# Kernel optimization log

Hardware: AMD Instinct MI355X
Metric: run time of the kernel (lower is better)

The kernel has to match this reference:

```python
import jax, jax.numpy as jnp
import numpy as np

B, H, NQ, NK, D = 256, 16, 49, 49, 64
SCALE = 1.0 / np.sqrt(D).astype(np.float32)
EPS = 1e-9  # matches kernel's 1/(l + 1e-9)


def setup_inputs() -> dict:
    key = jax.random.key(0)
    kq, kk, kv = jax.random.split(key, 3)
    q = jax.random.normal(kq, (B, H, NQ, D), dtype=jnp.float32)
    k = jax.random.normal(kk, (B, H, NK, D), dtype=jnp.float32)
    v = jax.random.normal(kv, (B, H, NK, D), dtype=jnp.float32)
    return {"q": q, "k": k, "v": v}


def reference(q, k, v):
    # scores: [B,H,Nq,Nk]
    s = jnp.einsum("bhqd,bhkd->bhqk", q, k) * SCALE
    m = jnp.max(s, axis=-1, keepdims=True)
    e = jnp.exp(s - m)
    l = jnp.sum(e, axis=-1, keepdims=True)
    p = e / (l + EPS)  # kernel divides by (l + 1e-9)
    out = jnp.einsum("bhqk,bhkd->bhqd", p, v)
    return out
```

## Files before the change

### kernel.cpp

```cpp
#include <hip/hip_runtime.h>


#define NQA 49
#define DD  64
#define ST  72

typedef __bf16 bf16x4 __attribute__((ext_vector_type(4)));
typedef __bf16 bf16x8 __attribute__((ext_vector_type(8)));
typedef float  f32x4  __attribute__((ext_vector_type(4)));

__device__ __forceinline__ int vt_off(int d, int k) {
    return d * ST + ((((k >> 3) + ((d >> 2) & 7)) & 7) << 3) + (k & 7);
}

__global__ __launch_bounds__(256, 5)
void attn49_kernel(const float* __restrict__ Q, const float* __restrict__ K,
                   const float* __restrict__ V, float* __restrict__ O) {
    __shared__ __bf16 Qs[64 * ST];
    __shared__ __bf16 Ks[64 * ST];
    __shared__ __bf16 Vt[64 * ST];

    const int tid = threadIdx.x;
    const size_t base = (size_t)blockIdx.x * (NQA * DD);
    const float* Qg = Q + base;
    const float* Kg = K + base;
    const float* Vg = V + base;

    {
        const int f  = tid & 15;
        const int r0 = tid >> 4;
        #pragma unroll
        for (int it = 0; it < 4; ++it) {
            const int r = r0 + 16 * it;
            float4 qv = {0.f,0.f,0.f,0.f}, kv = {0.f,0.f,0.f,0.f},
                   vv = {0.f,0.f,0.f,0.f};
            if (r < NQA) {
                qv = *(const float4*)(Qg + r * DD + 4 * f);
                kv = *(const float4*)(Kg + r * DD + 4 * f);
                vv = *(const float4*)(Vg + r * DD + 4 * f);
            }
            bf16x4 qb = { (__bf16)(0.125f*qv.x), (__bf16)(0.125f*qv.y),
                          (__bf16)(0.125f*qv.z), (__bf16)(0.125f*qv.w) };
            bf16x4 kb = { (__bf16)kv.x, (__bf16)kv.y, (__bf16)kv.z, (__bf16)kv.w };
            *(bf16x4*)&Qs[r * ST + 4 * f] = qb;
            *(bf16x4*)&Ks[r * ST + 4 * f] = kb;
            Vt[vt_off(4*f + 0, r)] = (__bf16)vv.x;
            Vt[vt_off(4*f + 1, r)] = (__bf16)vv.y;
            Vt[vt_off(4*f + 2, r)] = (__bf16)vv.z;
            Vt[vt_off(4*f + 3, r)] = (__bf16)vv.w;
        }
    }
    __syncthreads();

    const int w  = tid >> 6;
    const int lr = tid & 15;
    const int lg = (tid >> 4) & 3;

    bf16x8 aq0 = *(const bf16x8*)&Qs[(16*w + lr) * ST      + 8*lg];
    bf16x8 aq1 = *(const bf16x8*)&Qs[(16*w + lr) * ST + 32 + 8*lg];
    f32x4 acc[4] = {};
    #pragma unroll
    for (int t = 0; t < 4; ++t) {
        bf16x8 b0 = *(const bf16x8*)&Ks[(16*t + lr) * ST      + 8*lg];
        bf16x8 b1 = *(const bf16x8*)&Ks[(16*t + lr) * ST + 32 + 8*lg];
        acc[t] = __builtin_amdgcn_mfma_f32_16x16x32_bf16(aq0, b0, acc[t], 0, 0, 0);
        acc[t] = __builtin_amdgcn_mfma_f32_16x16x32_bf16(aq1, b1, acc[t], 0, 0, 0);
    }

    float inv_l[4];
    #pragma unroll
    for (int i = 0; i < 4; ++i) {
        const int gq = 16*w + 4*lg + i;
        float e0 = __expf(acc[0][i]);
        float e1 = __expf(acc[1][i]);
        float e2 = __expf(acc[2][i]);
        float e3 = (lr == 0) ? __expf(acc[3][i]) : 0.f;
        float sum = (e0 + e1) + (e2 + e3);
        #pragma unroll
        for (int d = 1; d < 16; d <<= 1) sum += __shfl_xor(sum, d, 64);
        inv_l[i] = 1.f / (sum + 1e-9f);
        Qs[gq * ST +  0 + lr] = (__bf16)e0;
        Qs[gq * ST + 16 + lr] = (__bf16)e1;
        Qs[gq * ST + 32 + lr] = (__bf16)e2;
        Qs[gq * ST + 48 + lr] = (__bf16)e3;
    }

    bf16x8 ap0 = *(const bf16x8*)&Qs[(16*w + lr) * ST      + 8*lg];
    bf16x8 ap1 = *(const bf16x8*)&Qs[(16*w + lr) * ST + 32 + 8*lg];
    f32x4 oacc[4] = {};
    #pragma unroll
    for (int t = 0; t < 4; ++t) {
        bf16x8 b0 = *(const bf16x8*)&Vt[vt_off(16*t + lr,  8*lg)];
        bf16x8 b1 = *(const bf16x8*)&Vt[vt_off(16*t + lr, 32 + 8*lg)];
        oacc[t] = __builtin_amdgcn_mfma_f32_16x16x32_bf16(ap0, b0, oacc[t], 0, 0, 0);
        oacc[t] = __builtin_amdgcn_mfma_f32_16x16x32_bf16(ap1, b1, oacc[t], 0, 0, 0);
    }

    float* Og = O + base;
    #pragma unroll
    for (int i = 0; i < 4; ++i) {
        const int gq = 16*w + 4*lg + i;
        if (gq < NQA) {
            #pragma unroll
            for (int t = 0; t < 4; ++t)
                Og[gq * DD + 16*t + lr] = oacc[t][i] * inv_l[i];
        }
    }
}

extern "C" void kernel_launch(void* const* d_in, const int* in_sizes, int n_in,
                              void* d_out, int out_size, void* d_ws, size_t ws_size,
                              hipStream_t stream) {
    const float* q = (const float*)d_in[0];
    const float* k = (const float*)d_in[1];
    const float* v = (const float*)d_in[2];
    float* out = (float*)d_out;
    (void)in_sizes; (void)n_in; (void)out_size; (void)d_ws; (void)ws_size;
    attn49_kernel<<<dim3(4096), dim3(256), 0, stream>>>(q, k, v, out);
}
```

Measured before the change: 186.4 us.

## Load Q directly into MFMA registers and reuse K buffer for probabilities

Q is now read from global memory straight into the MFMA A-operand registers instead of being staged through shared memory. The K shared buffer is reused for the exponentiated scores after a new barrier. This cuts LDS per block from three tiles to two, and the launch bound is raised from 5 to 8 blocks per CU to turn the saved LDS into higher occupancy. The cost is an extra __syncthreads and per-lane strided global Q loads that are less coalesced than before.

```diff
diff --git a/kernel.cpp b/kernel.cpp
--- a/kernel.cpp
+++ b/kernel.cpp
@@ -13,16 +13,14 @@
     return d * ST + ((((k >> 3) + ((d >> 2) & 7)) & 7) << 3) + (k & 7);
 }
 
-__global__ __launch_bounds__(256, 5)
+__global__ __launch_bounds__(256, 8)
 void attn49_kernel(const float* __restrict__ Q, const float* __restrict__ K,
                    const float* __restrict__ V, float* __restrict__ O) {
-    __shared__ __bf16 Qs[64 * ST];
-    __shared__ __bf16 Ks[64 * ST];
+    __shared__ __bf16 KPs[64 * ST];
     __shared__ __bf16 Vt[64 * ST];
 
     const int tid = threadIdx.x;
     const size_t base = (size_t)blockIdx.x * (NQA * DD);
-    const float* Qg = Q + base;
     const float* Kg = K + base;
     const float* Vg = V + base;
 
@@ -32,40 +30,57 @@
         #pragma unroll
         for (int it = 0; it < 4; ++it) {
             const int r = r0 + 16 * it;
-            float4 qv = {0.f,0.f,0.f,0.f}, kv = {0.f,0.f,0.f,0.f},
-                   vv = {0.f,0.f,0.f,0.f};
+            float4 kv = {0.f,0.f,0.f,0.f}, vv = {0.f,0.f,0.f,0.f};
             if (r < NQA) {
-                qv = *(const float4*)(Qg + r * DD + 4 * f);
                 kv = *(const float4*)(Kg + r * DD + 4 * f);
                 vv = *(const float4*)(Vg + r * DD + 4 * f);
             }
-            bf16x4 qb = { (__bf16)(0.125f*qv.x), (__bf16)(0.125f*qv.y),
-                          (__bf16)(0.125f*qv.z), (__bf16)(0.125f*qv.w) };
             bf16x4 kb = { (__bf16)kv.x, (__bf16)kv.y, (__bf16)kv.z, (__bf16)kv.w };
-            *(bf16x4*)&Qs[r * ST + 4 * f] = qb;
-            *(bf16x4*)&Ks[r * ST + 4 * f] = kb;
+            *(bf16x4*)&KPs[r * ST + 4 * f] = kb;
             Vt[vt_off(4*f + 0, r)] = (__bf16)vv.x;
             Vt[vt_off(4*f + 1, r)] = (__bf16)vv.y;
             Vt[vt_off(4*f + 2, r)] = (__bf16)vv.z;
             Vt[vt_off(4*f + 3, r)] = (__bf16)vv.w;
         }
     }
-    __syncthreads();
 
     const int w  = tid >> 6;
     const int lr = tid & 15;
     const int lg = (tid >> 4) & 3;
 
-    bf16x8 aq0 = *(const bf16x8*)&Qs[(16*w + lr) * ST      + 8*lg];
-    bf16x8 aq1 = *(const bf16x8*)&Qs[(16*w + lr) * ST + 32 + 8*lg];
+    bf16x8 aq0, aq1;
+    {
+        const int qrow = 16*w + lr;
+        float4 qa = {0.f,0.f,0.f,0.f}, qb = {0.f,0.f,0.f,0.f},
+               qc = {0.f,0.f,0.f,0.f}, qd = {0.f,0.f,0.f,0.f};
+        if (qrow < NQA) {
+            const float* Qr = Q + base + (size_t)qrow * DD + 8 * lg;
+            qa = *(const float4*)(Qr +  0);
+            qb = *(const float4*)(Qr +  4);
+            qc = *(const float4*)(Qr + 32);
+            qd = *(const float4*)(Qr + 36);
+        }
+        aq0 = bf16x8{ (__bf16)(0.125f*qa.x), (__bf16)(0.125f*qa.y),
+                      (__bf16)(0.125f*qa.z), (__bf16)(0.125f*qa.w),
+                      (__bf16)(0.125f*qb.x), (__bf16)(0.125f*qb.y),
+                      (__bf16)(0.125f*qb.z), (__bf16)(0.125f*qb.w) };
+        aq1 = bf16x8{ (__bf16)(0.125f*qc.x), (__bf16)(0.125f*qc.y),
+                      (__bf16)(0.125f*qc.z), (__bf16)(0.125f*qc.w),
+                      (__bf16)(0.125f*qd.x), (__bf16)(0.125f*qd.y),
+                      (__bf16)(0.125f*qd.z), (__bf16)(0.125f*qd.w) };
+    }
+    __syncthreads();
+
     f32x4 acc[4] = {};
     #pragma unroll
     for (int t = 0; t < 4; ++t) {
-        bf16x8 b0 = *(const bf16x8*)&Ks[(16*t + lr) * ST      + 8*lg];
-        bf16x8 b1 = *(const bf16x8*)&Ks[(16*t + lr) * ST + 32 + 8*lg];
+        bf16x8 b0 = *(const bf16x8*)&KPs[(16*t + lr) * ST      + 8*lg];
+        bf16x8 b1 = *(const bf16x8*)&KPs[(16*t + lr) * ST + 32 + 8*lg];
         acc[t] = __builtin_amdgcn_mfma_f32_16x16x32_bf16(aq0, b0, acc[t], 0, 0, 0);
         acc[t] = __builtin_amdgcn_mfma_f32_16x16x32_bf16(aq1, b1, acc[t], 0, 0, 0);
     }
+
+    __syncthreads();
 
     float inv_l[4];
     #pragma unroll
@@ -79,14 +94,14 @@
         #pragma unroll
         for (int d = 1; d < 16; d <<= 1) sum += __shfl_xor(sum, d, 64);
         inv_l[i] = 1.f / (sum + 1e-9f);
-        Qs[gq * ST +  0 + lr] = (__bf16)e0;
-        Qs[gq * ST + 16 + lr] = (__bf16)e1;
-        Qs[gq * ST + 32 + lr] = (__bf16)e2;
-        Qs[gq * ST + 48 + lr] = (__bf16)e3;
+        KPs[gq * ST +  0 + lr] = (__bf16)e0;
+        KPs[gq * ST + 16 + lr] = (__bf16)e1;
+        KPs[gq * ST + 32 + lr] = (__bf16)e2;
+        KPs[gq * ST + 48 + lr] = (__bf16)e3;
     }
 
-    bf16x8 ap0 = *(const bf16x8*)&Qs[(16*w + lr) * ST      + 8*lg];
-    bf16x8 ap1 = *(const bf16x8*)&Qs[(16*w + lr) * ST + 32 + 8*lg];
+    bf16x8 ap0 = *(const bf16x8*)&KPs[(16*w + lr) * ST      + 8*lg];
+    bf16x8 ap1 = *(const bf16x8*)&KPs[(16*w + lr) * ST + 32 + 8*lg];
     f32x4 oacc[4] = {};
     #pragma unroll
     for (int t = 0; t < 4; ++t) {
```

Result: no change. 184.9 us (-0.8%).

## Process four heads per block with double-buffered LDS and register prefetch

Applied to the files above, without the earlier changes.

Each block now handles four heads instead of one, and the grid shrinks to a quarter. Global loads for the next head are issued into registers while the current head computes, with K/V staged into alternating LDS buffers. Q is loaded straight into MFMA operand registers, so the Q shared buffer is gone and P is written into the K buffer after a barrier. The point is to hide global load latency and cut per-block launch and setup overhead, at the cost of higher register pressure and fewer concurrent blocks (launch bounds drop from 5 to 4).

```diff
diff --git a/kernel.cpp b/kernel.cpp
--- a/kernel.cpp
+++ b/kernel.cpp
@@ -4,6 +4,7 @@
 #define NQA 49
 #define DD  64
 #define ST  72
+#define HPB 4
 
 typedef __bf16 bf16x4 __attribute__((ext_vector_type(4)));
 typedef __bf16 bf16x8 __attribute__((ext_vector_type(8)));
@@ -13,59 +14,82 @@
     return d * ST + ((((k >> 3) + ((d >> 2) & 7)) & 7) << 3) + (k & 7);
 }
 
-__global__ __launch_bounds__(256, 5)
-void attn49_kernel(const float* __restrict__ Q, const float* __restrict__ K,
-                   const float* __restrict__ V, float* __restrict__ O) {
-    __shared__ __bf16 Qs[64 * ST];
-    __shared__ __bf16 Ks[64 * ST];
-    __shared__ __bf16 Vt[64 * ST];
+__device__ __forceinline__ void lds_barrier() {
+    asm volatile("s_waitcnt lgkmcnt(0)" ::: "memory");
+    __builtin_amdgcn_s_barrier();
+}
 
-    const int tid = threadIdx.x;
-    const size_t base = (size_t)blockIdx.x * (NQA * DD);
-    const float* Qg = Q + base;
+struct Pref {
+    float4 kr[4], vr[4];
+    float4 qa, qb, qc, qd;
+};
+
+__device__ __forceinline__ void issue_loads(const float* __restrict__ Q,
+                                            const float* __restrict__ K,
+                                            const float* __restrict__ V,
+                                            size_t head, int f, int r0,
+                                            int w, int lr, int lg, Pref& p) {
+    const size_t base = head * (size_t)(NQA * DD);
     const float* Kg = K + base;
     const float* Vg = V + base;
-
-    {
-        const int f  = tid & 15;
-        const int r0 = tid >> 4;
-        #pragma unroll
-        for (int it = 0; it < 4; ++it) {
-            const int r = r0 + 16 * it;
-            float4 qv = {0.f,0.f,0.f,0.f}, kv = {0.f,0.f,0.f,0.f},
-                   vv = {0.f,0.f,0.f,0.f};
-            if (r < NQA) {
-                qv = *(const float4*)(Qg + r * DD + 4 * f);
-                kv = *(const float4*)(Kg + r * DD + 4 * f);
-                vv = *(const float4*)(Vg + r * DD + 4 * f);
-            }
-            bf16x4 qb = { (__bf16)(0.125f*qv.x), (__bf16)(0.125f*qv.y),
-                          (__bf16)(0.125f*qv.z), (__bf16)(0.125f*qv.w) };
-            bf16x4 kb = { (__bf16)kv.x, (__bf16)kv.y, (__bf16)kv.z, (__bf16)kv.w };
-            *(bf16x4*)&Qs[r * ST + 4 * f] = qb;
-            *(bf16x4*)&Ks[r * ST + 4 * f] = kb;
-            Vt[vt_off(4*f + 0, r)] = (__bf16)vv.x;
-            Vt[vt_off(4*f + 1, r)] = (__bf16)vv.y;
-            Vt[vt_off(4*f + 2, r)] = (__bf16)vv.z;
-            Vt[vt_off(4*f + 3, r)] = (__bf16)vv.w;
+    #pragma unroll
+    for (int it = 0; it < 4; ++it) {
+        const int r = r0 + 16 * it;
+        p.kr[it] = float4{0.f, 0.f, 0.f, 0.f};
+        p.vr[it] = float4{0.f, 0.f, 0.f, 0.f};
+        if (r < NQA) {
+            p.kr[it] = *(const float4*)(Kg + r * DD + 4 * f);
+            p.vr[it] = *(const float4*)(Vg + r * DD + 4 * f);
         }
     }
-    __syncthreads();
+    const int qrow = 16 * w + lr;
+    p.qa = p.qb = p.qc = p.qd = float4{0.f, 0.f, 0.f, 0.f};
+    if (qrow < NQA) {
+        const float* Qr = Q + base + (size_t)qrow * DD + 8 * lg;
+        p.qa = *(const float4*)(Qr + 0);
+        p.qb = *(const float4*)(Qr + 4);
+        p.qc = *(const float4*)(Qr + 32);
+        p.qd = *(const float4*)(Qr + 36);
+    }
+}
 
-    const int w  = tid >> 6;
-    const int lr = tid & 15;
-    const int lg = (tid >> 4) & 3;
+__device__ __forceinline__ void stage(const Pref& p, __bf16* Ksb, __bf16* Vtb,
+                                      int f, int r0, bf16x8& aq0, bf16x8& aq1) {
+    #pragma unroll
+    for (int it = 0; it < 4; ++it) {
+        const int r = r0 + 16 * it;
+        bf16x4 kb = { (__bf16)p.kr[it].x, (__bf16)p.kr[it].y,
+                      (__bf16)p.kr[it].z, (__bf16)p.kr[it].w };
+        *(bf16x4*)&Ksb[r * ST + 4 * f] = kb;
+        Vtb[vt_off(4*f + 0, r)] = (__bf16)p.vr[it].x;
+        Vtb[vt_off(4*f + 1, r)] = (__bf16)p.vr[it].y;
+        Vtb[vt_off(4*f + 2, r)] = (__bf16)p.vr[it].z;
+        Vtb[vt_off(4*f + 3, r)] = (__bf16)p.vr[it].w;
+    }
+    aq0 = bf16x8{ (__bf16)(0.125f*p.qa.x), (__bf16)(0.125f*p.qa.y),
+                  (__bf16)(0.125f*p.qa.z), (__bf16)(0.125f*p.qa.w),
+                  (__bf16)(0.125f*p.qb.x), (__bf16)(0.125f*p.qb.y),
+                  (__bf16)(0.125f*p.qb.z), (__bf16)(0.125f*p.qb.w) };
+    aq1 = bf16x8{ (__bf16)(0.125f*p.qc.x), (__bf16)(0.125f*p.qc.y),
+                  (__bf16)(0.125f*p.qc.z), (__bf16)(0.125f*p.qc.w),
+                  (__bf16)(0.125f*p.qd.x), (__bf16)(0.125f*p.qd.y),
+                  (__bf16)(0.125f*p.qd.z), (__bf16)(0.125f*p.qd.w) };
+}
 
-    bf16x8 aq0 = *(const bf16x8*)&Qs[(16*w + lr) * ST      + 8*lg];
-    bf16x8 aq1 = *(const bf16x8*)&Qs[(16*w + lr) * ST + 32 + 8*lg];
+__device__ __forceinline__ void compute_head(float* __restrict__ O, size_t head,
+                                             __bf16* Ksb, const __bf16* Vtb,
+                                             bf16x8 aq0, bf16x8 aq1,
+                                             int w, int lr, int lg) {
     f32x4 acc[4] = {};
     #pragma unroll
     for (int t = 0; t < 4; ++t) {
-        bf16x8 b0 = *(const bf16x8*)&Ks[(16*t + lr) * ST      + 8*lg];
-        bf16x8 b1 = *(const bf16x8*)&Ks[(16*t + lr) * ST + 32 + 8*lg];
+        bf16x8 b0 = *(const bf16x8*)&Ksb[(16*t + lr) * ST      + 8*lg];
+        bf16x8 b1 = *(const bf16x8*)&Ksb[(16*t + lr) * ST + 32 + 8*lg];
         acc[t] = __builtin_amdgcn_mfma_f32_16x16x32_bf16(aq0, b0, acc[t], 0, 0, 0);
         acc[t] = __builtin_amdgcn_mfma_f32_16x16x32_bf16(aq1, b1, acc[t], 0, 0, 0);
     }
+
+    lds_barrier();
 
     float inv_l[4];
     #pragma unroll
@@ -79,24 +103,24 @@
         #pragma unroll
         for (int d = 1; d < 16; d <<= 1) sum += __shfl_xor(sum, d, 64);
         inv_l[i] = 1.f / (sum + 1e-9f);
-        Qs[gq * ST +  0 + lr] = (__bf16)e0;
-        Qs[gq * ST + 16 + lr] = (__bf16)e1;
-        Qs[gq * ST + 32 + lr] = (__bf16)e2;
-        Qs[gq * ST + 48 + lr] = (__bf16)e3;
+        Ksb[gq * ST +  0 + lr] = (__bf16)e0;
+        Ksb[gq * ST + 16 + lr] = (__bf16)e1;
+        Ksb[gq * ST + 32 + lr] = (__bf16)e2;
+        Ksb[gq * ST + 48 + lr] = (__bf16)e3;
     }
 
-    bf16x8 ap0 = *(const bf16x8*)&Qs[(16*w + lr) * ST      + 8*lg];
-    bf16x8 ap1 = *(const bf16x8*)&Qs[(16*w + lr) * ST + 32 + 8*lg];
+    bf16x8 ap0 = *(const bf16x8*)&Ksb[(16*w + lr) * ST      + 8*lg];
+    bf16x8 ap1 = *(const bf16x8*)&Ksb[(16*w + lr) * ST + 32 + 8*lg];
     f32x4 oacc[4] = {};
     #pragma unroll
     for (int t = 0; t < 4; ++t) {
-        bf16x8 b0 = *(const bf16x8*)&Vt[vt_off(16*t + lr,  8*lg)];
-        bf16x8 b1 = *(const bf16x8*)&Vt[vt_off(16*t + lr, 32 + 8*lg)];
+        bf16x8 b0 = *(const bf16x8*)&Vtb[vt_off(16*t + lr,  8*lg)];
+        bf16x8 b1 = *(const bf16x8*)&Vtb[vt_off(16*t + lr, 32 + 8*lg)];
         oacc[t] = __builtin_amdgcn_mfma_f32_16x16x32_bf16(ap0, b0, oacc[t], 0, 0, 0);
         oacc[t] = __builtin_amdgcn_mfma_f32_16x16x32_bf16(ap1, b1, oacc[t], 0, 0, 0);
     }
 
-    float* Og = O + base;
+    float* Og = O + head * (size_t)(NQA * DD);
     #pragma unroll
     for (int i = 0; i < 4; ++i) {
         const int gq = 16*w + 4*lg + i;
@@ -108,6 +132,46 @@
     }
 }
 
+__global__ __launch_bounds__(256, 4)
+void attn49_kernel(const float* __restrict__ Q, const float* __restrict__ K,
+                   const float* __restrict__ V, float* __restrict__ O) {
+    __shared__ __bf16 Ks[2][64 * ST];
+    __shared__ __bf16 Vt[2][64 * ST];
+
+    const int tid = threadIdx.x;
+    const int f  = tid & 15;
+    const int r0 = tid >> 4;
+    const int w  = tid >> 6;
+    const int lr = tid & 15;
+    const int lg = (tid >> 4) & 3;
+
+    const size_t h0 = (size_t)blockIdx.x * HPB;
+
+    Pref p;
+    bf16x8 aqA0, aqA1, aqB0, aqB1;
+
+    issue_loads(Q, K, V, h0 + 0, f, r0, w, lr, lg, p);
+    stage(p, Ks[0], Vt[0], f, r0, aqA0, aqA1);
+    issue_loads(Q, K, V, h0 + 1, f, r0, w, lr, lg, p);
+    lds_barrier();
+
+    compute_head(O, h0 + 0, Ks[0], Vt[0], aqA0, aqA1, w, lr, lg);
+    stage(p, Ks[1], Vt[1], f, r0, aqB0, aqB1);
+    issue_loads(Q, K, V, h0 + 2, f, r0, w, lr, lg, p);
+    lds_barrier();
+
+    compute_head(O, h0 + 1, Ks[1], Vt[1], aqB0, aqB1, w, lr, lg);
+    stage(p, Ks[0], Vt[0], f, r0, aqA0, aqA1);
+    issue_loads(Q, K, V, h0 + 3, f, r0, w, lr, lg, p);
+    lds_barrier();
+
+    compute_head(O, h0 + 2, Ks[0], Vt[0], aqA0, aqA1, w, lr, lg);
+    stage(p, Ks[1], Vt[1], f, r0, aqB0, aqB1);
+    lds_barrier();
+
+    compute_head(O, h0 + 3, Ks[1], Vt[1], aqB0, aqB1, w, lr, lg);
+}
+
 extern "C" void kernel_launch(void* const* d_in, const int* in_sizes, int n_in,
                               void* d_out, int out_size, void* d_ws, size_t ws_size,
                               hipStream_t stream) {
@@ -116,5 +180,5 @@
     const float* v = (const float*)d_in[2];
     float* out = (float*)d_out;
     (void)in_sizes; (void)n_in; (void)out_size; (void)d_ws; (void)ws_size;
-    attn49_kernel<<<dim3(4096), dim3(256), 0, stream>>>(q, k, v, out);
+    attn49_kernel<<<dim3(4096 / HPB), dim3(256), 0, stream>>>(q, k, v, out);
 }
```

After: 190.3 us. 2.1% more time.

## Load Q/K/V directly into MFMA registers, drop shared-memory staging and barrier

Applied to the files above, without the earlier changes.

Replaces block-wide shared-memory staging of Q, K and transposed V with per-wave direct global loads converted into bf16 MFMA operands, keeping only a small per-wave LDS tile for the probability matrix. This removes the block barrier and LDS traffic and lowers shared memory per block. In exchange each wave re-reads all of K and V from global/L2 and V is gathered with scalar strided loads. Launch bounds are also changed to target 4 blocks per SIMD.

```diff
diff --git a/kernel.cpp b/kernel.cpp
--- a/kernel.cpp
+++ b/kernel.cpp
@@ -3,107 +3,114 @@
 
 #define NQA 49
 #define DD  64
-#define ST  72
+#define PST 72
 
-typedef __bf16 bf16x4 __attribute__((ext_vector_type(4)));
 typedef __bf16 bf16x8 __attribute__((ext_vector_type(8)));
 typedef float  f32x4  __attribute__((ext_vector_type(4)));
 
-__device__ __forceinline__ int vt_off(int d, int k) {
-    return d * ST + ((((k >> 3) + ((d >> 2) & 7)) & 7) << 3) + (k & 7);
-}
-
-__global__ __launch_bounds__(256, 5)
+__global__ __launch_bounds__(256, 4)
 void attn49_kernel(const float* __restrict__ Q, const float* __restrict__ K,
                    const float* __restrict__ V, float* __restrict__ O) {
-    __shared__ __bf16 Qs[64 * ST];
-    __shared__ __bf16 Ks[64 * ST];
-    __shared__ __bf16 Vt[64 * ST];
+    __shared__ __bf16 P[4][16 * PST];
 
     const int tid = threadIdx.x;
+    const int w  = tid >> 6;
+    const int lr = tid & 15;
+    const int lg = (tid >> 4) & 3;
+
     const size_t base = (size_t)blockIdx.x * (NQA * DD);
     const float* Qg = Q + base;
     const float* Kg = K + base;
     const float* Vg = V + base;
 
+    bf16x8 aq0, aq1;
     {
-        const int f  = tid & 15;
-        const int r0 = tid >> 4;
-        #pragma unroll
-        for (int it = 0; it < 4; ++it) {
-            const int r = r0 + 16 * it;
-            float4 qv = {0.f,0.f,0.f,0.f}, kv = {0.f,0.f,0.f,0.f},
-                   vv = {0.f,0.f,0.f,0.f};
-            if (r < NQA) {
-                qv = *(const float4*)(Qg + r * DD + 4 * f);
-                kv = *(const float4*)(Kg + r * DD + 4 * f);
-                vv = *(const float4*)(Vg + r * DD + 4 * f);
-            }
-            bf16x4 qb = { (__bf16)(0.125f*qv.x), (__bf16)(0.125f*qv.y),
-                          (__bf16)(0.125f*qv.z), (__bf16)(0.125f*qv.w) };
-            bf16x4 kb = { (__bf16)kv.x, (__bf16)kv.y, (__bf16)kv.z, (__bf16)kv.w };
-            *(bf16x4*)&Qs[r * ST + 4 * f] = qb;
-            *(bf16x4*)&Ks[r * ST + 4 * f] = kb;
-            Vt[vt_off(4*f + 0, r)] = (__bf16)vv.x;
-            Vt[vt_off(4*f + 1, r)] = (__bf16)vv.y;
-            Vt[vt_off(4*f + 2, r)] = (__bf16)vv.z;
-            Vt[vt_off(4*f + 3, r)] = (__bf16)vv.w;
-        }
+        const int qrow = 16*w + lr;
+        const int qc   = (qrow < NQA) ? qrow : (NQA - 1);
+        const float* Qr = Qg + qc * DD + 8 * lg;
+        float4 a = *(const float4*)(Qr + 0);
+        float4 b = *(const float4*)(Qr + 4);
+        float4 c = *(const float4*)(Qr + 32);
+        float4 d = *(const float4*)(Qr + 36);
+        aq0 = bf16x8{ (__bf16)(0.125f*a.x), (__bf16)(0.125f*a.y),
+                      (__bf16)(0.125f*a.z), (__bf16)(0.125f*a.w),
+                      (__bf16)(0.125f*b.x), (__bf16)(0.125f*b.y),
+                      (__bf16)(0.125f*b.z), (__bf16)(0.125f*b.w) };
+        aq1 = bf16x8{ (__bf16)(0.125f*c.x), (__bf16)(0.125f*c.y),
+                      (__bf16)(0.125f*c.z), (__bf16)(0.125f*c.w),
+                      (__bf16)(0.125f*d.x), (__bf16)(0.125f*d.y),
+                      (__bf16)(0.125f*d.z), (__bf16)(0.125f*d.w) };
     }
-    __syncthreads();
 
-    const int w  = tid >> 6;
-    const int lr = tid & 15;
-    const int lg = (tid >> 4) & 3;
-
-    bf16x8 aq0 = *(const bf16x8*)&Qs[(16*w + lr) * ST      + 8*lg];
-    bf16x8 aq1 = *(const bf16x8*)&Qs[(16*w + lr) * ST + 32 + 8*lg];
     f32x4 acc[4] = {};
     #pragma unroll
     for (int t = 0; t < 4; ++t) {
-        bf16x8 b0 = *(const bf16x8*)&Ks[(16*t + lr) * ST      + 8*lg];
-        bf16x8 b1 = *(const bf16x8*)&Ks[(16*t + lr) * ST + 32 + 8*lg];
-        acc[t] = __builtin_amdgcn_mfma_f32_16x16x32_bf16(aq0, b0, acc[t], 0, 0, 0);
-        acc[t] = __builtin_amdgcn_mfma_f32_16x16x32_bf16(aq1, b1, acc[t], 0, 0, 0);
+        const int kr = 16*t + lr;
+        const int kc = (kr < NQA) ? kr : (NQA - 1);
+        const float* Kr = Kg + kc * DD + 8 * lg;
+        float4 a = *(const float4*)(Kr + 0);
+        float4 b = *(const float4*)(Kr + 4);
+        float4 c = *(const float4*)(Kr + 32);
+        float4 d = *(const float4*)(Kr + 36);
+        bf16x8 kb0 = { (__bf16)a.x, (__bf16)a.y, (__bf16)a.z, (__bf16)a.w,
+                       (__bf16)b.x, (__bf16)b.y, (__bf16)b.z, (__bf16)b.w };
+        bf16x8 kb1 = { (__bf16)c.x, (__bf16)c.y, (__bf16)c.z, (__bf16)c.w,
+                       (__bf16)d.x, (__bf16)d.y, (__bf16)d.z, (__bf16)d.w };
+        acc[t] = __builtin_amdgcn_mfma_f32_16x16x32_bf16(aq0, kb0, acc[t], 0, 0, 0);
+        acc[t] = __builtin_amdgcn_mfma_f32_16x16x32_bf16(aq1, kb1, acc[t], 0, 0, 0);
     }
 
+    __bf16* Pw = &P[w][0];
     float inv_l[4];
     #pragma unroll
-    for (int i = 0; i < 4; ++i) {
-        const int gq = 16*w + 4*lg + i;
-        float e0 = __expf(acc[0][i]);
-        float e1 = __expf(acc[1][i]);
-        float e2 = __expf(acc[2][i]);
-        float e3 = (lr == 0) ? __expf(acc[3][i]) : 0.f;
+    for (int ii = 0; ii < 4; ++ii) {
+        float e0 = __expf(acc[0][ii]);
+        float e1 = __expf(acc[1][ii]);
+        float e2 = __expf(acc[2][ii]);
+        float e3 = (lr == 0) ? __expf(acc[3][ii]) : 0.f;
         float sum = (e0 + e1) + (e2 + e3);
         #pragma unroll
         for (int d = 1; d < 16; d <<= 1) sum += __shfl_xor(sum, d, 64);
-        inv_l[i] = 1.f / (sum + 1e-9f);
-        Qs[gq * ST +  0 + lr] = (__bf16)e0;
-        Qs[gq * ST + 16 + lr] = (__bf16)e1;
-        Qs[gq * ST + 32 + lr] = (__bf16)e2;
-        Qs[gq * ST + 48 + lr] = (__bf16)e3;
+        inv_l[ii] = 1.f / (sum + 1e-9f);
+        const int pr = 4*lg + ii;
+        Pw[pr * PST +  0 + lr] = (__bf16)e0;
+        Pw[pr * PST + 16 + lr] = (__bf16)e1;
+        Pw[pr * PST + 32 + lr] = (__bf16)e2;
+        Pw[pr * PST + 48 + lr] = (__bf16)e3;
     }
 
-    bf16x8 ap0 = *(const bf16x8*)&Qs[(16*w + lr) * ST      + 8*lg];
-    bf16x8 ap1 = *(const bf16x8*)&Qs[(16*w + lr) * ST + 32 + 8*lg];
+    bf16x8 ap0 = *(const bf16x8*)&Pw[lr * PST      + 8*lg];
+    bf16x8 ap1 = *(const bf16x8*)&Pw[lr * PST + 32 + 8*lg];
+
+    int voff[16];
+    #pragma unroll
+    for (int u = 0; u < 16; ++u) {
+        const int vr = 32 * (u >> 3) + 8 * lg + (u & 7);
+        voff[u] = ((vr < NQA) ? vr : (NQA - 1)) * DD;
+    }
     f32x4 oacc[4] = {};
     #pragma unroll
     for (int t = 0; t < 4; ++t) {
-        bf16x8 b0 = *(const bf16x8*)&Vt[vt_off(16*t + lr,  8*lg)];
-        bf16x8 b1 = *(const bf16x8*)&Vt[vt_off(16*t + lr, 32 + 8*lg)];
-        oacc[t] = __builtin_amdgcn_mfma_f32_16x16x32_bf16(ap0, b0, oacc[t], 0, 0, 0);
-        oacc[t] = __builtin_amdgcn_mfma_f32_16x16x32_bf16(ap1, b1, oacc[t], 0, 0, 0);
+        const float* Vc = Vg + 16*t + lr;
+        #pragma unroll
+        for (int h = 0; h < 2; ++h) {
+            bf16x8 vb;
+            #pragma unroll
+            for (int j = 0; j < 8; ++j)
+                vb[j] = (__bf16)Vc[voff[8*h + j]];
+            oacc[t] = __builtin_amdgcn_mfma_f32_16x16x32_bf16(
+                          h ? ap1 : ap0, vb, oacc[t], 0, 0, 0);
+        }
     }
 
     float* Og = O + base;
     #pragma unroll
-    for (int i = 0; i < 4; ++i) {
-        const int gq = 16*w + 4*lg + i;
+    for (int ii = 0; ii < 4; ++ii) {
+        const int gq = 16*w + 4*lg + ii;
         if (gq < NQA) {
             #pragma unroll
             for (int t = 0; t < 4; ++t)
-                Og[gq * DD + 16*t + lr] = oacc[t][i] * inv_l[i];
+                Og[gq * DD + 16*t + lr] = oacc[t][ii] * inv_l[ii];
         }
     }
 }
```

New measurement: 186.2 us. About the same (-0.1%).
